# Optimization experiments

Hardware: AMD Instinct MI355X
Metric: run time of the kernel (lower is better)

## Reference

```python
import jax, jax.numpy as jnp
import numpy as np

N = 50000
E = 800000
NFEAT = 256
NHID = 64
HEADS = 4
NCLASS = 16
NEG_SLOPE = 0.2


def setup_inputs() -> dict:
    key = jax.random.key(0)
    ks = jax.random.split(key, 12)
    g = lambda k, s, scale: (jax.random.normal(k, s, dtype=jnp.float32) * scale)
    inp = {
        "x": g(ks[0], (N, NFEAT), 1.0),
        "src": jax.random.randint(ks[1], (E,), 0, N, dtype=jnp.int32),
        "dst": jax.random.randint(ks[2], (E,), 0, N, dtype=jnp.int32),
        # layer 1 params (DGL GATConv: fc no-bias, attn_l/attn_r, output bias)
        "W1": g(ks[3], (NFEAT, HEADS * NHID), (2.0 / NFEAT) ** 0.5),
        "al1": g(ks[4], (HEADS, NHID), 0.1),
        "ar1": g(ks[5], (HEADS, NHID), 0.1),
        "b1": jnp.zeros((HEADS * NHID,), dtype=jnp.float32),
        # layer 2 params (1 head)
        "W2": g(ks[6], (HEADS * NHID, NCLASS), (2.0 / (HEADS * NHID)) ** 0.5),
        "al2": g(ks[7], (1, NCLASS), 0.1),
        "ar2": g(ks[8], (1, NCLASS), 0.1),
        "b2": jnp.zeros((NCLASS,), dtype=jnp.float32),
    }
    return inp


def gat_conv(x, src, dst, W, al, ar, b, heads, dh):
    # x: [N, Fin] -> feat: [N, H, D]
    n = x.shape[0]
    feat = (x @ W).reshape(n, heads, dh)
    el = jnp.einsum("nhd,hd->nh", feat, al)  # [N, H]
    er = jnp.einsum("nhd,hd->nh", feat, ar)
    e = jax.nn.leaky_relu(el[src] + er[dst], NEG_SLOPE)  # [E, H]
    # segment softmax over destination nodes
    emax = jax.ops.segment_max(e, dst, num_segments=n)
    emax = jnp.where(jnp.isfinite(emax), emax, jnp.float32(0.0))
    ex = jnp.exp(e - emax[dst])  # [E, H]
    denom = jax.ops.segment_sum(ex, dst, num_segments=n)  # [N, H]
    alpha = ex / denom[dst]  # [E, H]
    # gather src feats, weight, scatter-add to dst
    msg = feat[src] * alpha[:, :, None]  # [E, H, D]
    out = jax.ops.segment_sum(msg, dst, num_segments=n)  # [N, H, D]
    return out + b.reshape(1, heads, dh)


def reference(x, src, dst, W1, al1, ar1, b1, W2, al2, ar2, b2):
    h = gat_conv(x, src, dst, W1, al1, ar1, b1, HEADS, NHID)  # [N, 4, nhid]
    h = h.reshape(N, HEADS * NHID)
    h = jax.nn.elu(h)
    h = gat_conv(h, src, dst, W2, al2, ar2, b2, 1, NCLASS)  # [N, 1, nclass]
    h = h.reshape(N, NCLASS)
    return jax.nn.log_softmax(h, axis=1)
```

## Files before the change

### kernel.cpp

```cpp
#include <hip/hip_runtime.h>
#include <hip/hip_bf16.h>

#define N_NODES 50000
#define NP1     50001
#define N_EDGES 800000
#define NFEAT   256
#define NHID    64
#define HEADS   4
#define NCLASS  16
#define NEG_SLOPE 0.2f

#define NBLK  782
#define NBUCK 196
#define NSCAN (NBUCK * NBLK)
#define NSCB  150
#define MAXB  5120

typedef __attribute__((ext_vector_type(8))) short short8;
typedef __attribute__((ext_vector_type(4))) float floatx4;
typedef __attribute__((ext_vector_type(2))) float floatx2;

__device__ __forceinline__ float blo(unsigned int u) { return __uint_as_float(u << 16); }
__device__ __forceinline__ float bhi(unsigned int u) { return __uint_as_float(u & 0xffff0000u); }
__device__ __forceinline__ float b2f(unsigned short u) {
    return __uint_as_float(((unsigned int)u) << 16);
}
__device__ __forceinline__ unsigned short f2b(float f) {
    unsigned int x = __float_as_uint(f);
    unsigned int r = x + 0x7fffu + ((x >> 16) & 1u);
    return (unsigned short)(r >> 16);
}
__device__ __forceinline__ unsigned int pack2(float a, float b) {
    return (unsigned int)f2b(a) | ((unsigned int)f2b(b) << 16);
}
__device__ __forceinline__ float leaky(float x) { return fmaxf(x, NEG_SLOPE * x); }

__device__ __forceinline__ void fp8acc(uint4 u, float ex, float* acc) {
    floatx2 p;
    p = __builtin_amdgcn_cvt_pk_f32_fp8(u.x, 0); acc[0]  = fmaf(p[0], ex, acc[0]);  acc[1]  = fmaf(p[1], ex, acc[1]);
    p = __builtin_amdgcn_cvt_pk_f32_fp8(u.x, 1); acc[2]  = fmaf(p[0], ex, acc[2]);  acc[3]  = fmaf(p[1], ex, acc[3]);
    p = __builtin_amdgcn_cvt_pk_f32_fp8(u.y, 0); acc[4]  = fmaf(p[0], ex, acc[4]);  acc[5]  = fmaf(p[1], ex, acc[5]);
    p = __builtin_amdgcn_cvt_pk_f32_fp8(u.y, 1); acc[6]  = fmaf(p[0], ex, acc[6]);  acc[7]  = fmaf(p[1], ex, acc[7]);
    p = __builtin_amdgcn_cvt_pk_f32_fp8(u.z, 0); acc[8]  = fmaf(p[0], ex, acc[8]);  acc[9]  = fmaf(p[1], ex, acc[9]);
    p = __builtin_amdgcn_cvt_pk_f32_fp8(u.z, 1); acc[10] = fmaf(p[0], ex, acc[10]); acc[11] = fmaf(p[1], ex, acc[11]);
    p = __builtin_amdgcn_cvt_pk_f32_fp8(u.w, 0); acc[12] = fmaf(p[0], ex, acc[12]); acc[13] = fmaf(p[1], ex, acc[13]);
    p = __builtin_amdgcn_cvt_pk_f32_fp8(u.w, 1); acc[14] = fmaf(p[0], ex, acc[14]); acc[15] = fmaf(p[1], ex, acc[15]);
}

__global__ __launch_bounds__(256) void p1_kernel(
        const int* __restrict__ dst, int* __restrict__ bhist,
        const float* __restrict__ W1, const float* __restrict__ W2,
        const float* __restrict__ al1, const float* __restrict__ ar1,
        unsigned short* __restrict__ W1E, unsigned short* __restrict__ W2T) {
    __shared__ float tile[64][65];
    __shared__ int hist[NBUCK];
    int b = blockIdx.x, t = threadIdx.x;
    if (b < NBLK) {
        if (t < NBUCK) hist[t] = 0;
        __syncthreads();
        int e = (b * 256 + t) * 4;
        if (e < N_EDGES) {
            int4 d = *(const int4*)&dst[e];
            atomicAdd(&hist[d.x >> 8], 1);
            atomicAdd(&hist[d.y >> 8], 1);
            atomicAdd(&hist[d.z >> 8], 1);
            atomicAdd(&hist[d.w >> 8], 1);
        }
        __syncthreads();
        if (t < NBUCK) bhist[t * NBLK + b] = hist[t];
        return;
    }
    int pb = b - NBLK;
    if (pb < 16) {
        int tk = (pb & 3) * 64, tn = (pb >> 2) * 64;
        int tx = t & 63, ty = t >> 6;
#pragma unroll
        for (int r = 0; r < 16; ++r) {
            int row = ty * 16 + r;
            tile[row][tx] = W1[(tk + row) * 256 + tn + tx];
        }
        __syncthreads();
#pragma unroll
        for (int r = 0; r < 16; ++r) {
            int row = ty * 16 + r;
            W1E[(tn + row) * 256 + tk + tx] = f2b(tile[tx][row]);
        }
    } else if (pb < 20) {
        int h = pb - 16;
        int w = t >> 6, lane = t & 63;
        float alv = al1[h * 64 + lane];
        float arv = ar1[h * 64 + lane];
        for (int k = w; k < 256; k += 4) {
            float wv = W1[k * 256 + h * 64 + lane];
            float sl = wv * alv, sr = wv * arv;
#pragma unroll
            for (int off = 1; off < 64; off <<= 1) {
                sl += __shfl_xor(sl, off);
                sr += __shfl_xor(sr, off);
            }
            if (lane == 0) {
                W1E[(256 + h) * 256 + k] = f2b(sl);
                W1E[(260 + h) * 256 + k] = f2b(sr);
            }
        }
    } else {
        int n = t >> 4, k0 = (t & 15) * 16;
#pragma unroll
        for (int j = 0; j < 16; ++j)
            W2T[n * 256 + k0 + j] = f2b(W2[(k0 + j) * 16 + n]);
#pragma unroll
        for (int j = 0; j < 8; ++j)
            W1E[264 * 256 + j * 256 + t] = 0;
    }
}

__global__ __launch_bounds__(256) void scanA_kernel(const int* __restrict__ bhist,
                                                    int* __restrict__ partial,
                                                    int* __restrict__ bsum) {
    __shared__ int wsum[4];
    int t = threadIdx.x;
    int base = blockIdx.x * 1024 + t * 4;
    int v0 = (base + 0 < NSCAN) ? bhist[base + 0] : 0;
    int v1 = (base + 1 < NSCAN) ? bhist[base + 1] : 0;
    int v2 = (base + 2 < NSCAN) ? bhist[base + 2] : 0;
    int v3 = (base + 3 < NSCAN) ? bhist[base + 3] : 0;
    int s = v0 + v1 + v2 + v3;
    int lane = t & 63, w = t >> 6;
    int incl = s;
#pragma unroll
    for (int off = 1; off < 64; off <<= 1) {
        int x = __shfl_up(incl, off);
        if (lane >= off) incl += x;
    }
    if (lane == 63) wsum[w] = incl;
    __syncthreads();
    int woff = 0;
    for (int k = 0; k < w; ++k) woff += wsum[k];
    int excl = woff + incl - s;
    if (base + 0 < NSCAN) partial[base + 0] = excl;
    if (base + 1 < NSCAN) partial[base + 1] = excl + v0;
    if (base + 2 < NSCAN) partial[base + 2] = excl + v0 + v1;
    if (base + 3 < NSCAN) partial[base + 3] = excl + v0 + v1 + v2;
    if (t == 255) bsum[blockIdx.x] = woff + incl;
}

__global__ __launch_bounds__(256) void p2_kernel(const int* __restrict__ src,
                                                 const int* __restrict__ dst,
                                                 const int* __restrict__ partial,
                                                 const int* __restrict__ bsum,
                                                 unsigned int* __restrict__ ebuf) {
    __shared__ int wsum[4];
    __shared__ int sb[256];
    __shared__ int bs[NBUCK];
    __shared__ int lcnt[256];
    __shared__ int lofs[256];
    __shared__ int lfill[256];
    __shared__ unsigned int sorted[1024];
    int b = blockIdx.x, t = threadIdx.x;
    int lane = t & 63, w = t >> 6;
    {
        int v = (t < NSCB) ? bsum[t] : 0;
        int incl = v;
#pragma unroll
        for (int off = 1; off < 64; off <<= 1) {
            int x = __shfl_up(incl, off);
            if (lane >= off) incl += x;
        }
        if (lane == 63) wsum[w] = incl;
        __syncthreads();
        int woff = 0;
        for (int k = 0; k < w; ++k) woff += wsum[k];
        sb[t] = woff + incl - v;
    }
    lcnt[t] = 0;
    __syncthreads();
    if (t < NBUCK) {
        int idx = t * NBLK + b;
        bs[t] = partial[idx] + sb[idx >> 10];
    }
    int e = (b * 256 + t) * 4;
    int4 d, s;
    bool valid = e < N_EDGES;
    if (valid) {
        d = *(const int4*)&dst[e];
        s = *(const int4*)&src[e];
        atomicAdd(&lcnt[d.x >> 8], 1);
        atomicAdd(&lcnt[d.y >> 8], 1);
        atomicAdd(&lcnt[d.z >> 8], 1);
        atomicAdd(&lcnt[d.w >> 8], 1);
    }
    __syncthreads();
    {
        int v = lcnt[t];
        int incl = v;
#pragma unroll
        for (int off = 1; off < 64; off <<= 1) {
            int x = __shfl_up(incl, off);
            if (lane >= off) incl += x;
        }
        if (lane == 63) wsum[w] = incl;
        __syncthreads();
        int woff = 0;
        for (int k = 0; k < w; ++k) woff += wsum[k];
        int excl = woff + incl - v;
        lofs[t] = excl;
        lfill[t] = excl;
    }
    __syncthreads();
    if (valid) {
        int p0 = atomicAdd(&lfill[d.x >> 8], 1);
        sorted[p0] = ((unsigned int)s.x << 16) | (unsigned int)d.x;
        int p1 = atomicAdd(&lfill[d.y >> 8], 1);
        sorted[p1] = ((unsigned int)s.y << 16) | (unsigned int)d.y;
        int p2 = atomicAdd(&lfill[d.z >> 8], 1);
        sorted[p2] = ((unsigned int)s.z << 16) | (unsigned int)d.z;
        int p3 = atomicAdd(&lfill[d.w >> 8], 1);
        sorted[p3] = ((unsigned int)s.w << 16) | (unsigned int)d.w;
    }
    __syncthreads();
    int ve = min(1024, N_EDGES - b * 1024);
    for (int i = t; i < ve; i += 256) {
        unsigned int p = sorted[i];
        int k = (p & 0xFFFFu) >> 8;
        ebuf[bs[k] + (i - lofs[k])] = p;
    }
}

__global__ __launch_bounds__(256) void p3_kernel(const int* __restrict__ partial,
                                                 const int* __restrict__ bsum,
                                                 const unsigned int* __restrict__ ebuf,
                                                 int* __restrict__ row_ptr,
                                                 int* __restrict__ csr_src) {
    __shared__ int wsum[4];
    __shared__ int sb[256];
    __shared__ int lcnt[256];
    __shared__ int lfill[256];
    __shared__ int sorted[MAXB];
    int b = blockIdx.x, t = threadIdx.x;
    int lane = t & 63, w = t >> 6;
    {
        int v = (t < NSCB) ? bsum[t] : 0;
        int incl = v;
#pragma unroll
        for (int off = 1; off < 64; off <<= 1) {
            int x = __shfl_up(incl, off);
            if (lane >= off) incl += x;
        }
        if (lane == 63) wsum[w] = incl;
        __syncthreads();
        int woff = 0;
        for (int k = 0; k < w; ++k) woff += wsum[k];
        sb[t] = woff + incl - v;
    }
    __syncthreads();
    int i0 = b * NBLK;
    int base = partial[i0] + sb[i0 >> 10];
    int endb;
    if (b == NBUCK - 1) endb = N_EDGES;
    else {
        int i1 = (b + 1) * NBLK;
        endb = partial[i1] + sb[i1 >> 10];
    }
    lcnt[t] = 0;
    __syncthreads();
    for (int i = base + t; i < endb; i += 256)
        atomicAdd(&lcnt[ebuf[i] & 255u], 1);
    __syncthreads();
    {
        int v = lcnt[t];
        int incl = v;
#pragma unroll
        for (int off = 1; off < 64; off <<= 1) {
            int x = __shfl_up(incl, off);
            if (lane >= off) incl += x;
        }
        if (lane == 63) wsum[w] = incl;
        __syncthreads();
        int woff = 0;
        for (int k = 0; k < w; ++k) woff += wsum[k];
        int excl = woff + incl - v;
        lfill[t] = excl;
        int node = b * 256 + t;
        if (node < NP1) row_ptr[node] = base + excl;
    }
    __syncthreads();
    for (int i = base + t; i < endb; i += 256) {
        unsigned int p = ebuf[i];
        int pos = atomicAdd(&lfill[p & 255u], 1);
        sorted[pos] = (int)(p >> 16);
    }
    __syncthreads();
    int M = endb - base;
    for (int i = t; i < M; i += 256)
        csr_src[base + i] = sorted[i];
}

__global__ __launch_bounds__(256, 2) void gemm1_mfma_kernel(
        const float* __restrict__ X, const unsigned short* __restrict__ BT,
        unsigned char* __restrict__ C, float* __restrict__ el, float* __restrict__ er) {
    __shared__ __align__(16) unsigned short As[128 * 40];
    __shared__ __align__(16) unsigned short Bs[272 * 40];
    int t = threadIdx.x;
    int m0 = blockIdx.x * 128;
    int lane = t & 63, wm = t >> 6;
    int quad = lane >> 4, l16 = lane & 15;

    floatx4 acc[2][17];
#pragma unroll
    for (int i = 0; i < 2; ++i)
#pragma unroll
        for (int j = 0; j < 17; ++j) acc[i][j] = (floatx4){0.f, 0.f, 0.f, 0.f};

    int arow = t >> 1, ak = (t & 1) * 16;
    int grow = m0 + arow;
    const float* xrow = X + (size_t)grow * 256 + ak;

    for (int k0 = 0; k0 < 256; k0 += 32) {
        float4 v0 = make_float4(0.f, 0.f, 0.f, 0.f), v1 = v0, v2 = v0, v3 = v0;
        if (grow < N_NODES) {
            v0 = *(const float4*)(xrow + k0 + 0);
            v1 = *(const float4*)(xrow + k0 + 4);
            v2 = *(const float4*)(xrow + k0 + 8);
            v3 = *(const float4*)(xrow + k0 + 12);
        }
        uint4 p0, p1;
        p0.x = pack2(v0.x, v0.y); p0.y = pack2(v0.z, v0.w);
        p0.z = pack2(v1.x, v1.y); p0.w = pack2(v1.z, v1.w);
        p1.x = pack2(v2.x, v2.y); p1.y = pack2(v2.z, v2.w);
        p1.z = pack2(v3.x, v3.y); p1.w = pack2(v3.z, v3.w);
        *(uint4*)&As[arow * 40 + ak] = p0;
        *(uint4*)&As[arow * 40 + ak + 8] = p1;
#pragma unroll
        for (int i = 0; i < 5; ++i) {
            int ch = t + i * 256;
            if (ch < 1088) {
                int row = ch >> 2, off = (ch & 3) * 8;
                *(uint4*)&Bs[row * 40 + off] = *(const uint4*)(BT + row * 256 + k0 + off);
            }
        }
        __syncthreads();

        short8 a0 = *(const short8*)&As[(wm * 32 + l16) * 40 + quad * 8];
        short8 a1 = *(const short8*)&As[(wm * 32 + 16 + l16) * 40 + quad * 8];
#pragma unroll
        for (int nf = 0; nf < 17; ++nf) {
            short8 bb = *(const short8*)&Bs[(nf * 16 + l16) * 40 + quad * 8];
            acc[0][nf] = __builtin_amdgcn_mfma_f32_16x16x32_bf16(a0, bb, acc[0][nf], 0, 0, 0);
            acc[1][nf] = __builtin_amdgcn_mfma_f32_16x16x32_bf16(a1, bb, acc[1][nf], 0, 0, 0);
        }
        __syncthreads();
    }

#pragma unroll
    for (int mf = 0; mf < 2; ++mf) {
#pragma unroll
        for (int r = 0; r < 4; ++r) {
            int row = m0 + wm * 32 + mf * 16 + quad * 4 + r;
            if (row < N_NODES && l16 < 8) {
                float v = acc[mf][16][r];
                if (l16 < 4) el[row * 4 + l16] = v;
                else er[row * 4 + (l16 - 4)] = v;
            }
        }
    }

    unsigned short* scr = Bs + wm * 1536;
    int half = lane >> 5, l32 = lane & 31;
    int rrow = l32 >> 1, coff = (l32 & 1) * 8;
#pragma unroll
    for (int mf = 0; mf < 2; ++mf) {
#pragma unroll
        for (int p = 0; p < 8; ++p) {
            unsigned short* base = scr + (p & 1) * 768;
#pragma unroll
            for (int fr = 0; fr < 2; ++fr) {
                int nf = 2 * p + fr;
                unsigned short* fb = base + fr * 384;
#pragma unroll
                for (int r = 0; r < 4; ++r)
                    fb[(quad * 4 + r) * 24 + l16] = f2b(acc[mf][nf][r]);
            }
            uint4 val = *(const uint4*)(base + half * 384 + rrow * 24 + coff);
            int row = m0 + wm * 32 + mf * 16 + rrow;
            int nf = 2 * p + half;
            if (row < N_NODES) {
                float f0 = blo(val.x), f1 = bhi(val.x), f2 = blo(val.y), f3 = bhi(val.y);
                float f4 = blo(val.z), f5 = bhi(val.z), f6 = blo(val.w), f7 = bhi(val.w);
                int lo = __builtin_amdgcn_cvt_pk_fp8_f32(f0, f1, 0, 0);
                lo = __builtin_amdgcn_cvt_pk_fp8_f32(f2, f3, lo, 1);
                int hi = __builtin_amdgcn_cvt_pk_fp8_f32(f4, f5, 0, 0);
                hi = __builtin_amdgcn_cvt_pk_fp8_f32(f6, f7, hi, 1);
                uint2 o;
                o.x = (unsigned int)lo;
                o.y = (unsigned int)hi;
                *(uint2*)&C[(size_t)row * 256 + nf * 16 + coff] = o;
            }
        }
    }
}

__global__ void agg1_kernel(const unsigned char* __restrict__ feat1,
                            const float* __restrict__ el, const float* __restrict__ er,
                            const int* __restrict__ row_ptr, const int* __restrict__ csr_src,
                            const float* __restrict__ b1, unsigned short* __restrict__ h1b) {
    int wave = threadIdx.x >> 6, lane = threadIdx.x & 63;
    int n = blockIdx.x * 4 + wave;
    if (n >= N_NODES) return;
    int q = lane >> 4, l16 = lane & 15;
    int h = l16 >> 2;
    float er_h = er[n * 4 + h];
    int start = row_ptr[n], end = row_ptr[n + 1];

    float acc[16];
#pragma unroll
    for (int j = 0; j < 16; ++j) acc[j] = 0.f;
    float denom = 0.f;

    int i = start + q;
    for (; i + 4 < end; i += 8) {
        int s0 = csr_src[i];
        int s1 = csr_src[i + 4];
        float ex0 = __expf(leaky(el[s0 * 4 + h] + er_h));
        float ex1 = __expf(leaky(el[s1 * 4 + h] + er_h));
        uint4 a = *(const uint4*)(feat1 + (size_t)s0 * 256 + l16 * 16);
        uint4 b = *(const uint4*)(feat1 + (size_t)s1 * 256 + l16 * 16);
        denom += ex0 + ex1;
        fp8acc(a, ex0, acc);
        fp8acc(b, ex1, acc);
    }
    if (i < end) {
        int s = csr_src[i];
        float ex = __expf(leaky(el[s * 4 + h] + er_h));
        uint4 u = *(const uint4*)(feat1 + (size_t)s * 256 + l16 * 16);
        denom += ex;
        fp8acc(u, ex, acc);
    }
#pragma unroll
    for (int j = 0; j < 16; ++j) {
        acc[j] += __shfl_xor(acc[j], 16);
        acc[j] += __shfl_xor(acc[j], 32);
    }
    denom += __shfl_xor(denom, 16);
    denom += __shfl_xor(denom, 32);

    if (q == 0) {
        float inv = (end > start) ? 1.f / denom : 0.f;
        float o[16];
#pragma unroll
        for (int j = 0; j < 16; j += 4) {
            float4 b4 = *(const float4*)&b1[l16 * 16 + j];
            o[j + 0] = fmaf(acc[j + 0], inv, b4.x);
            o[j + 1] = fmaf(acc[j + 1], inv, b4.y);
            o[j + 2] = fmaf(acc[j + 2], inv, b4.z);
            o[j + 3] = fmaf(acc[j + 3], inv, b4.w);
        }
#pragma unroll
        for (int j = 0; j < 16; ++j) o[j] = o[j] > 0.f ? o[j] : __expf(o[j]) - 1.f;
        uint4 pa, pb;
        pa.x = pack2(o[0], o[1]);   pa.y = pack2(o[2], o[3]);
        pa.z = pack2(o[4], o[5]);   pa.w = pack2(o[6], o[7]);
        pb.x = pack2(o[8], o[9]);   pb.y = pack2(o[10], o[11]);
        pb.z = pack2(o[12], o[13]); pb.w = pack2(o[14], o[15]);
        uint4* dstp = (uint4*)(h1b + (size_t)n * 256 + l16 * 16);
        dstp[0] = pa;
        dstp[1] = pb;
    }
}

__global__ __launch_bounds__(256) void gemm2_mfma_kernel(
        const unsigned short* __restrict__ h1b, const unsigned short* __restrict__ W2T,
        const float* __restrict__ al2, const float* __restrict__ ar2,
        unsigned short* __restrict__ feat2b, float* __restrict__ el2, float* __restrict__ er2) {
    int wave = threadIdx.x >> 6, lane = threadIdx.x & 63;
    int l16 = lane & 15, quad = lane >> 4;
    int row0 = (blockIdx.x * 4 + wave) * 16;
    if (row0 >= N_NODES) return;
    floatx4 acc = (floatx4){0.f, 0.f, 0.f, 0.f};
    const unsigned short* arow = h1b + (size_t)(row0 + l16) * 256 + quad * 8;
    const unsigned short* brow = W2T + (size_t)l16 * 256 + quad * 8;
#pragma unroll
    for (int k0 = 0; k0 < 256; k0 += 32) {
        short8 a = *(const short8*)(arow + k0);
        short8 b = *(const short8*)(brow + k0);
        acc = __builtin_amdgcn_mfma_f32_16x16x32_bf16(a, b, acc, 0, 0, 0);
    }
    float a2 = al2[l16], r2 = ar2[l16];
#pragma unroll
    for (int r = 0; r < 4; ++r) {
        int row = row0 + quad * 4 + r;
        float v = acc[r];
        feat2b[row * 16 + l16] = f2b(v);
        float pl = v * a2, pr = v * r2;
#pragma unroll
        for (int off = 1; off < 16; off <<= 1) {
            pl += __shfl_xor(pl, off);
            pr += __shfl_xor(pr, off);
        }
        if (l16 == 0) {
            el2[row] = pl;
            er2[row] = pr;
        }
    }
}

__global__ void agg2_kernel(const unsigned short* __restrict__ feat2b,
                            const float* __restrict__ el2, const float* __restrict__ er2,
                            const int* __restrict__ row_ptr, const int* __restrict__ csr_src,
                            const float* __restrict__ b2, float* __restrict__ out) {
    int wave = threadIdx.x >> 6, lane = threadIdx.x & 63;
    int n = blockIdx.x * 4 + wave;
    if (n >= N_NODES) return;
    int start = row_ptr[n], end = row_ptr[n + 1];
    float ern = er2[n];
    int eo = lane >> 4, c = lane & 15;
    float acc = 0.f, denom = 0.f;
    int i = start + eo;
    for (; i + 4 < end; i += 8) {
        int s0 = csr_src[i], s1 = csr_src[i + 4];
        float ex0 = __expf(leaky(el2[s0] + ern));
        float ex1 = __expf(leaky(el2[s1] + ern));
        float f0 = b2f(feat2b[s0 * 16 + c]), f1 = b2f(feat2b[s1 * 16 + c]);
        denom += ex0 + ex1;
        acc = fmaf(f0, ex0, acc);
        acc = fmaf(f1, ex1, acc);
    }
    if (i < end) {
        int s = csr_src[i];
        float ex = __expf(leaky(el2[s] + ern));
        denom += ex;
        acc = fmaf(b2f(feat2b[s * 16 + c]), ex, acc);
    }
    acc += __shfl_xor(acc, 16);
    acc += __shfl_xor(acc, 32);
    denom += __shfl_xor(denom, 16);
    denom += __shfl_xor(denom, 32);
    float v = ((end > start) ? acc / denom : 0.f) + b2[c];
    float mx = v;
#pragma unroll
    for (int off = 1; off < 16; off <<= 1) mx = fmaxf(mx, __shfl_xor(mx, off));
    float ex2 = __expf(v - mx);
    float s2 = ex2;
#pragma unroll
    for (int off = 1; off < 16; off <<= 1) s2 += __shfl_xor(s2, off);
    float res = v - mx - logf(s2);
    if (lane < 16) out[n * 16 + lane] = res;
}

extern "C" void kernel_launch(void* const* d_in, const int* in_sizes, int n_in,
                              void* d_out, int out_size, void* d_ws, size_t ws_size,
                              hipStream_t stream) {
    const float* x   = (const float*)d_in[0];
    const int*   src = (const int*)d_in[1];
    const int*   dst = (const int*)d_in[2];
    const float* W1  = (const float*)d_in[3];
    const float* al1 = (const float*)d_in[4];
    const float* ar1 = (const float*)d_in[5];
    const float* b1  = (const float*)d_in[6];
    const float* W2  = (const float*)d_in[7];
    const float* al2 = (const float*)d_in[8];
    const float* ar2 = (const float*)d_in[9];
    const float* b2  = (const float*)d_in[10];
    float* out = (float*)d_out;

    char* ws = (char*)d_ws;
    size_t off = 0;
    auto alloc = [&](size_t bytes) -> void* {
        void* p = ws + off;
        off += (bytes + 255) & ~(size_t)255;
        return p;
    };
    unsigned short* W1E    = (unsigned short*)alloc((size_t)272 * 256 * 2);
    unsigned short* W2T    = (unsigned short*)alloc((size_t)16 * 256 * 2);
    unsigned char*  feat1  = (unsigned char*)alloc((size_t)N_NODES * 256);
    unsigned short* h1b    = (unsigned short*)alloc((size_t)N_NODES * 256 * 2);
    unsigned short* feat2b = (unsigned short*)alloc((size_t)N_NODES * 16 * 2);
    float* el1     = (float*)alloc((size_t)N_NODES * 4 * 4);
    float* er1     = (float*)alloc((size_t)N_NODES * 4 * 4);
    float* el2     = (float*)alloc((size_t)N_NODES * 4);
    float* er2     = (float*)alloc((size_t)N_NODES * 4);
    int*   bhist   = (int*)alloc((size_t)NSCAN * 4);
    int*   partial = (int*)alloc((size_t)NSCAN * 4);
    int*   bsum    = (int*)alloc((size_t)256 * 4);
    int*   row_ptr = (int*)alloc((size_t)NP1 * 4);
    unsigned int* ebuf = (unsigned int*)alloc((size_t)N_EDGES * 4);
    int*   csr_src = (int*)alloc((size_t)N_EDGES * 4);

    dim3 b256(256);
    p1_kernel<<<NBLK + 21, b256, 0, stream>>>(dst, bhist, W1, W2, al1, ar1, W1E, W2T);
    scanA_kernel<<<NSCB, b256, 0, stream>>>(bhist, partial, bsum);
    p2_kernel<<<NBLK, b256, 0, stream>>>(src, dst, partial, bsum, ebuf);
    p3_kernel<<<NBUCK, b256, 0, stream>>>(partial, bsum, ebuf, row_ptr, csr_src);

    gemm1_mfma_kernel<<<(N_NODES + 127) / 128, b256, 0, stream>>>(x, W1E, feat1, el1, er1);
    agg1_kernel<<<(N_NODES + 3) / 4, b256, 0, stream>>>(feat1, el1, er1, row_ptr, csr_src, b1, h1b);

    gemm2_mfma_kernel<<<(N_NODES + 63) / 64, b256, 0, stream>>>(h1b, W2T, al2, ar2, feat2b, el2, er2);
    agg2_kernel<<<(N_NODES + 3) / 4, b256, 0, stream>>>(feat2b, el2, er2, row_ptr, csr_src, b2, out);
}
```

Measured before the change: 247.6 us.

## Merge GEMM1 into edge-sort scatter kernel and pack FMAs in agg1

The layer-1 GEMM (x@W1 plus el/er) now runs in the same launch as the edge bucket-scatter pass. The first 391 blocks do the MFMA GEMM and the rest do the sort scatter, so the two independent stages overlap and one launch is removed. The agg1 accumulation now uses floatx2 elementwise FMA to encourage packed FMA instructions. The combined kernel carries the GEMM's larger shared-memory footprint in every block, which may lower occupancy for the scatter blocks.

```diff
diff --git a/kernel.cpp b/kernel.cpp
--- a/kernel.cpp
+++ b/kernel.cpp
@@ -15,6 +15,7 @@
 #define NSCAN (NBUCK * NBLK)
 #define NSCB  150
 #define MAXB  5120
+#define NGB   391
 
 typedef __attribute__((ext_vector_type(8))) short short8;
 typedef __attribute__((ext_vector_type(4))) float floatx4;
@@ -35,16 +36,15 @@
 }
 __device__ __forceinline__ float leaky(float x) { return fmaxf(x, NEG_SLOPE * x); }
 
-__device__ __forceinline__ void fp8acc(uint4 u, float ex, float* acc) {
-    floatx2 p;
-    p = __builtin_amdgcn_cvt_pk_f32_fp8(u.x, 0); acc[0]  = fmaf(p[0], ex, acc[0]);  acc[1]  = fmaf(p[1], ex, acc[1]);
-    p = __builtin_amdgcn_cvt_pk_f32_fp8(u.x, 1); acc[2]  = fmaf(p[0], ex, acc[2]);  acc[3]  = fmaf(p[1], ex, acc[3]);
-    p = __builtin_amdgcn_cvt_pk_f32_fp8(u.y, 0); acc[4]  = fmaf(p[0], ex, acc[4]);  acc[5]  = fmaf(p[1], ex, acc[5]);
-    p = __builtin_amdgcn_cvt_pk_f32_fp8(u.y, 1); acc[6]  = fmaf(p[0], ex, acc[6]);  acc[7]  = fmaf(p[1], ex, acc[7]);
-    p = __builtin_amdgcn_cvt_pk_f32_fp8(u.z, 0); acc[8]  = fmaf(p[0], ex, acc[8]);  acc[9]  = fmaf(p[1], ex, acc[9]);
-    p = __builtin_amdgcn_cvt_pk_f32_fp8(u.z, 1); acc[10] = fmaf(p[0], ex, acc[10]); acc[11] = fmaf(p[1], ex, acc[11]);
-    p = __builtin_amdgcn_cvt_pk_f32_fp8(u.w, 0); acc[12] = fmaf(p[0], ex, acc[12]); acc[13] = fmaf(p[1], ex, acc[13]);
-    p = __builtin_amdgcn_cvt_pk_f32_fp8(u.w, 1); acc[14] = fmaf(p[0], ex, acc[14]); acc[15] = fmaf(p[1], ex, acc[15]);
+__device__ __forceinline__ void fp8acc2(uint4 u, floatx2 exv, floatx2* acc) {
+    acc[0] = __builtin_elementwise_fma(__builtin_amdgcn_cvt_pk_f32_fp8(u.x, 0), exv, acc[0]);
+    acc[1] = __builtin_elementwise_fma(__builtin_amdgcn_cvt_pk_f32_fp8(u.x, 1), exv, acc[1]);
+    acc[2] = __builtin_elementwise_fma(__builtin_amdgcn_cvt_pk_f32_fp8(u.y, 0), exv, acc[2]);
+    acc[3] = __builtin_elementwise_fma(__builtin_amdgcn_cvt_pk_f32_fp8(u.y, 1), exv, acc[3]);
+    acc[4] = __builtin_elementwise_fma(__builtin_amdgcn_cvt_pk_f32_fp8(u.z, 0), exv, acc[4]);
+    acc[5] = __builtin_elementwise_fma(__builtin_amdgcn_cvt_pk_f32_fp8(u.z, 1), exv, acc[5]);
+    acc[6] = __builtin_elementwise_fma(__builtin_amdgcn_cvt_pk_f32_fp8(u.w, 0), exv, acc[6]);
+    acc[7] = __builtin_elementwise_fma(__builtin_amdgcn_cvt_pk_f32_fp8(u.w, 1), exv, acc[7]);
 }
 
 __global__ __launch_bounds__(256) void p1_kernel(
@@ -144,11 +144,14 @@
     if (t == 255) bsum[blockIdx.x] = woff + incl;
 }
 
-__global__ __launch_bounds__(256) void p2_kernel(const int* __restrict__ src,
-                                                 const int* __restrict__ dst,
-                                                 const int* __restrict__ partial,
-                                                 const int* __restrict__ bsum,
-                                                 unsigned int* __restrict__ ebuf) {
+__global__ __launch_bounds__(256, 2) void p2g1_kernel(
+        const int* __restrict__ src, const int* __restrict__ dst,
+        const int* __restrict__ partial, const int* __restrict__ bsum,
+        unsigned int* __restrict__ ebuf,
+        const float* __restrict__ X, const unsigned short* __restrict__ BT,
+        unsigned char* __restrict__ C, float* __restrict__ el, float* __restrict__ er) {
+    __shared__ __align__(16) unsigned short As[128 * 40];
+    __shared__ __align__(16) unsigned short Bs[272 * 40];
     __shared__ int wsum[4];
     __shared__ int sb[256];
     __shared__ int bs[NBUCK];
@@ -156,73 +159,175 @@
     __shared__ int lofs[256];
     __shared__ int lfill[256];
     __shared__ unsigned int sorted[1024];
-    int b = blockIdx.x, t = threadIdx.x;
-    int lane = t & 63, w = t >> 6;
-    {
-        int v = (t < NSCB) ? bsum[t] : 0;
-        int incl = v;
-#pragma unroll
-        for (int off = 1; off < 64; off <<= 1) {
-            int x = __shfl_up(incl, off);
-            if (lane >= off) incl += x;
-        }
-        if (lane == 63) wsum[w] = incl;
-        __syncthreads();
-        int woff = 0;
-        for (int k = 0; k < w; ++k) woff += wsum[k];
-        sb[t] = woff + incl - v;
-    }
-    lcnt[t] = 0;
-    __syncthreads();
-    if (t < NBUCK) {
-        int idx = t * NBLK + b;
-        bs[t] = partial[idx] + sb[idx >> 10];
-    }
-    int e = (b * 256 + t) * 4;
-    int4 d, s;
-    bool valid = e < N_EDGES;
-    if (valid) {
-        d = *(const int4*)&dst[e];
-        s = *(const int4*)&src[e];
-        atomicAdd(&lcnt[d.x >> 8], 1);
-        atomicAdd(&lcnt[d.y >> 8], 1);
-        atomicAdd(&lcnt[d.z >> 8], 1);
-        atomicAdd(&lcnt[d.w >> 8], 1);
-    }
-    __syncthreads();
-    {
-        int v = lcnt[t];
-        int incl = v;
-#pragma unroll
-        for (int off = 1; off < 64; off <<= 1) {
-            int x = __shfl_up(incl, off);
-            if (lane >= off) incl += x;
-        }
-        if (lane == 63) wsum[w] = incl;
-        __syncthreads();
-        int woff = 0;
-        for (int k = 0; k < w; ++k) woff += wsum[k];
-        int excl = woff + incl - v;
-        lofs[t] = excl;
-        lfill[t] = excl;
-    }
-    __syncthreads();
-    if (valid) {
-        int p0 = atomicAdd(&lfill[d.x >> 8], 1);
-        sorted[p0] = ((unsigned int)s.x << 16) | (unsigned int)d.x;
-        int p1 = atomicAdd(&lfill[d.y >> 8], 1);
-        sorted[p1] = ((unsigned int)s.y << 16) | (unsigned int)d.y;
-        int p2 = atomicAdd(&lfill[d.z >> 8], 1);
-        sorted[p2] = ((unsigned int)s.z << 16) | (unsigned int)d.z;
-        int p3 = atomicAdd(&lfill[d.w >> 8], 1);
-        sorted[p3] = ((unsigned int)s.w << 16) | (unsigned int)d.w;
-    }
-    __syncthreads();
-    int ve = min(1024, N_EDGES - b * 1024);
-    for (int i = t; i < ve; i += 256) {
-        unsigned int p = sorted[i];
-        int k = (p & 0xFFFFu) >> 8;
-        ebuf[bs[k] + (i - lofs[k])] = p;
+
+    int t = threadIdx.x;
+    if (blockIdx.x >= NGB) {
+        int b = blockIdx.x - NGB;
+        int lane = t & 63, w = t >> 6;
+        {
+            int v = (t < NSCB) ? bsum[t] : 0;
+            int incl = v;
+#pragma unroll
+            for (int off = 1; off < 64; off <<= 1) {
+                int x = __shfl_up(incl, off);
+                if (lane >= off) incl += x;
+            }
+            if (lane == 63) wsum[w] = incl;
+            __syncthreads();
+            int woff = 0;
+            for (int k = 0; k < w; ++k) woff += wsum[k];
+            sb[t] = woff + incl - v;
+        }
+        lcnt[t] = 0;
+        __syncthreads();
+        if (t < NBUCK) {
+            int idx = t * NBLK + b;
+            bs[t] = partial[idx] + sb[idx >> 10];
+        }
+        int e = (b * 256 + t) * 4;
+        int4 d, s;
+        bool valid = e < N_EDGES;
+        if (valid) {
+            d = *(const int4*)&dst[e];
+            s = *(const int4*)&src[e];
+            atomicAdd(&lcnt[d.x >> 8], 1);
+            atomicAdd(&lcnt[d.y >> 8], 1);
+            atomicAdd(&lcnt[d.z >> 8], 1);
+            atomicAdd(&lcnt[d.w >> 8], 1);
+        }
+        __syncthreads();
+        {
+            int v = lcnt[t];
+            int incl = v;
+#pragma unroll
+            for (int off = 1; off < 64; off <<= 1) {
+                int x = __shfl_up(incl, off);
+                if (lane >= off) incl += x;
+            }
+            if (lane == 63) wsum[w] = incl;
+            __syncthreads();
+            int woff = 0;
+            for (int k = 0; k < w; ++k) woff += wsum[k];
+            int excl = woff + incl - v;
+            lofs[t] = excl;
+            lfill[t] = excl;
+        }
+        __syncthreads();
+        if (valid) {
+            int p0 = atomicAdd(&lfill[d.x >> 8], 1);
+            sorted[p0] = ((unsigned int)s.x << 16) | (unsigned int)d.x;
+            int p1 = atomicAdd(&lfill[d.y >> 8], 1);
+            sorted[p1] = ((unsigned int)s.y << 16) | (unsigned int)d.y;
+            int p2 = atomicAdd(&lfill[d.z >> 8], 1);
+            sorted[p2] = ((unsigned int)s.z << 16) | (unsigned int)d.z;
+            int p3 = atomicAdd(&lfill[d.w >> 8], 1);
+            sorted[p3] = ((unsigned int)s.w << 16) | (unsigned int)d.w;
+        }
+        __syncthreads();
+        int ve = min(1024, N_EDGES - b * 1024);
+        for (int i = t; i < ve; i += 256) {
+            unsigned int p = sorted[i];
+            int k = (p & 0xFFFFu) >> 8;
+            ebuf[bs[k] + (i - lofs[k])] = p;
+        }
+        return;
+    }
+
+    int m0 = blockIdx.x * 128;
+    int lane = t & 63, wm = t >> 6;
+    int quad = lane >> 4, l16 = lane & 15;
+
+    floatx4 acc[2][17];
+#pragma unroll
+    for (int i = 0; i < 2; ++i)
+#pragma unroll
+        for (int j = 0; j < 17; ++j) acc[i][j] = (floatx4){0.f, 0.f, 0.f, 0.f};
+
+    int arow = t >> 1, ak = (t & 1) * 16;
+    int grow = m0 + arow;
+    const float* xrow = X + (size_t)grow * 256 + ak;
+
+    for (int k0 = 0; k0 < 256; k0 += 32) {
+        float4 v0 = make_float4(0.f, 0.f, 0.f, 0.f), v1 = v0, v2 = v0, v3 = v0;
+        if (grow < N_NODES) {
+            v0 = *(const float4*)(xrow + k0 + 0);
+            v1 = *(const float4*)(xrow + k0 + 4);
+            v2 = *(const float4*)(xrow + k0 + 8);
+            v3 = *(const float4*)(xrow + k0 + 12);
+        }
+        uint4 p0, p1;
+        p0.x = pack2(v0.x, v0.y); p0.y = pack2(v0.z, v0.w);
+        p0.z = pack2(v1.x, v1.y); p0.w = pack2(v1.z, v1.w);
+        p1.x = pack2(v2.x, v2.y); p1.y = pack2(v2.z, v2.w);
+        p1.z = pack2(v3.x, v3.y); p1.w = pack2(v3.z, v3.w);
+        *(uint4*)&As[arow * 40 + ak] = p0;
+        *(uint4*)&As[arow * 40 + ak + 8] = p1;
+#pragma unroll
+        for (int i = 0; i < 5; ++i) {
+            int ch = t + i * 256;
+            if (ch < 1088) {
+                int row = ch >> 2, off = (ch & 3) * 8;
+                *(uint4*)&Bs[row * 40 + off] = *(const uint4*)(BT + row * 256 + k0 + off);
+            }
+        }
+        __syncthreads();
+
+        short8 a0 = *(const short8*)&As[(wm * 32 + l16) * 40 + quad * 8];
+        short8 a1 = *(const short8*)&As[(wm * 32 + 16 + l16) * 40 + quad * 8];
+#pragma unroll
+        for (int nf = 0; nf < 17; ++nf) {
+            short8 bb = *(const short8*)&Bs[(nf * 16 + l16) * 40 + quad * 8];
+            acc[0][nf] = __builtin_amdgcn_mfma_f32_16x16x32_bf16(a0, bb, acc[0][nf], 0, 0, 0);
+            acc[1][nf] = __builtin_amdgcn_mfma_f32_16x16x32_bf16(a1, bb, acc[1][nf], 0, 0, 0);
+        }
+        __syncthreads();
+    }
+
+#pragma unroll
+    for (int mf = 0; mf < 2; ++mf) {
+#pragma unroll
+        for (int r = 0; r < 4; ++r) {
+            int row = m0 + wm * 32 + mf * 16 + quad * 4 + r;
+            if (row < N_NODES && l16 < 8) {
+                float v = acc[mf][16][r];
+                if (l16 < 4) el[row * 4 + l16] = v;
+                else er[row * 4 + (l16 - 4)] = v;
+            }
+        }
+    }
+
+    unsigned short* scr = Bs + wm * 1536;
+    int half = lane >> 5, l32 = lane & 31;
+    int rrow = l32 >> 1, coff = (l32 & 1) * 8;
+#pragma unroll
+    for (int mf = 0; mf < 2; ++mf) {
+#pragma unroll
+        for (int p = 0; p < 8; ++p) {
+            unsigned short* base = scr + (p & 1) * 768;
+#pragma unroll
+            for (int fr = 0; fr < 2; ++fr) {
+                int nf = 2 * p + fr;
+                unsigned short* fb = base + fr * 384;
+#pragma unroll
+                for (int r = 0; r < 4; ++r)
+                    fb[(quad * 4 + r) * 24 + l16] = f2b(acc[mf][nf][r]);
+            }
+            uint4 val = *(const uint4*)(base + half * 384 + rrow * 24 + coff);
+            int row = m0 + wm * 32 + mf * 16 + rrow;
+            int nf = 2 * p + half;
+            if (row < N_NODES) {
+                float f0 = blo(val.x), f1 = bhi(val.x), f2 = blo(val.y), f3 = bhi(val.y);
+                float f4 = blo(val.z), f5 = bhi(val.z), f6 = blo(val.w), f7 = bhi(val.w);
+                int lo = __builtin_amdgcn_cvt_pk_fp8_f32(f0, f1, 0, 0);
+                lo = __builtin_amdgcn_cvt_pk_fp8_f32(f2, f3, lo, 1);
+                int hi = __builtin_amdgcn_cvt_pk_fp8_f32(f4, f5, 0, 0);
+                hi = __builtin_amdgcn_cvt_pk_fp8_f32(f6, f7, hi, 1);
+                uint2 o;
+                o.x = (unsigned int)lo;
+                o.y = (unsigned int)hi;
+                *(uint2*)&C[(size_t)row * 256 + nf * 16 + coff] = o;
+            }
+        }
     }
 }
 
@@ -295,110 +400,6 @@
         csr_src[base + i] = sorted[i];
 }
 
-__global__ __launch_bounds__(256, 2) void gemm1_mfma_kernel(
-        const float* __restrict__ X, const unsigned short* __restrict__ BT,
-        unsigned char* __restrict__ C, float* __restrict__ el, float* __restrict__ er) {
-    __shared__ __align__(16) unsigned short As[128 * 40];
-    __shared__ __align__(16) unsigned short Bs[272 * 40];
-    int t = threadIdx.x;
-    int m0 = blockIdx.x * 128;
-    int lane = t & 63, wm = t >> 6;
-    int quad = lane >> 4, l16 = lane & 15;
-
-    floatx4 acc[2][17];
-#pragma unroll
-    for (int i = 0; i < 2; ++i)
-#pragma unroll
-        for (int j = 0; j < 17; ++j) acc[i][j] = (floatx4){0.f, 0.f, 0.f, 0.f};
-
-    int arow = t >> 1, ak = (t & 1) * 16;
-    int grow = m0 + arow;
-    const float* xrow = X + (size_t)grow * 256 + ak;
-
-    for (int k0 = 0; k0 < 256; k0 += 32) {
-        float4 v0 = make_float4(0.f, 0.f, 0.f, 0.f), v1 = v0, v2 = v0, v3 = v0;
-        if (grow < N_NODES) {
-            v0 = *(const float4*)(xrow + k0 + 0);
-            v1 = *(const float4*)(xrow + k0 + 4);
-            v2 = *(const float4*)(xrow + k0 + 8);
-            v3 = *(const float4*)(xrow + k0 + 12);
-        }
-        uint4 p0, p1;
-        p0.x = pack2(v0.x, v0.y); p0.y = pack2(v0.z, v0.w);
-        p0.z = pack2(v1.x, v1.y); p0.w = pack2(v1.z, v1.w);
-        p1.x = pack2(v2.x, v2.y); p1.y = pack2(v2.z, v2.w);
-        p1.z = pack2(v3.x, v3.y); p1.w = pack2(v3.z, v3.w);
-        *(uint4*)&As[arow * 40 + ak] = p0;
-        *(uint4*)&As[arow * 40 + ak + 8] = p1;
-#pragma unroll
-        for (int i = 0; i < 5; ++i) {
-            int ch = t + i * 256;
-            if (ch < 1088) {
-                int row = ch >> 2, off = (ch & 3) * 8;
-                *(uint4*)&Bs[row * 40 + off] = *(const uint4*)(BT + row * 256 + k0 + off);
-            }
-        }
-        __syncthreads();
-
-        short8 a0 = *(const short8*)&As[(wm * 32 + l16) * 40 + quad * 8];
-        short8 a1 = *(const short8*)&As[(wm * 32 + 16 + l16) * 40 + quad * 8];
-#pragma unroll
-        for (int nf = 0; nf < 17; ++nf) {
-            short8 bb = *(const short8*)&Bs[(nf * 16 + l16) * 40 + quad * 8];
-            acc[0][nf] = __builtin_amdgcn_mfma_f32_16x16x32_bf16(a0, bb, acc[0][nf], 0, 0, 0);
-            acc[1][nf] = __builtin_amdgcn_mfma_f32_16x16x32_bf16(a1, bb, acc[1][nf], 0, 0, 0);
-        }
-        __syncthreads();
-    }
-
-#pragma unroll
-    for (int mf = 0; mf < 2; ++mf) {
-#pragma unroll
-        for (int r = 0; r < 4; ++r) {
-            int row = m0 + wm * 32 + mf * 16 + quad * 4 + r;
-            if (row < N_NODES && l16 < 8) {
-                float v = acc[mf][16][r];
-                if (l16 < 4) el[row * 4 + l16] = v;
-                else er[row * 4 + (l16 - 4)] = v;
-            }
-        }
-    }
-
-    unsigned short* scr = Bs + wm * 1536;
-    int half = lane >> 5, l32 = lane & 31;
-    int rrow = l32 >> 1, coff = (l32 & 1) * 8;
-#pragma unroll
-    for (int mf = 0; mf < 2; ++mf) {
-#pragma unroll
-        for (int p = 0; p < 8; ++p) {
-            unsigned short* base = scr + (p & 1) * 768;
-#pragma unroll
-            for (int fr = 0; fr < 2; ++fr) {
-                int nf = 2 * p + fr;
-                unsigned short* fb = base + fr * 384;
-#pragma unroll
-                for (int r = 0; r < 4; ++r)
-                    fb[(quad * 4 + r) * 24 + l16] = f2b(acc[mf][nf][r]);
-            }
-            uint4 val = *(const uint4*)(base + half * 384 + rrow * 24 + coff);
-            int row = m0 + wm * 32 + mf * 16 + rrow;
-            int nf = 2 * p + half;
-            if (row < N_NODES) {
-                float f0 = blo(val.x), f1 = bhi(val.x), f2 = blo(val.y), f3 = bhi(val.y);
-                float f4 = blo(val.z), f5 = bhi(val.z), f6 = blo(val.w), f7 = bhi(val.w);
-                int lo = __builtin_amdgcn_cvt_pk_fp8_f32(f0, f1, 0, 0);
-                lo = __builtin_amdgcn_cvt_pk_fp8_f32(f2, f3, lo, 1);
-                int hi = __builtin_amdgcn_cvt_pk_fp8_f32(f4, f5, 0, 0);
-                hi = __builtin_amdgcn_cvt_pk_fp8_f32(f6, f7, hi, 1);
-                uint2 o;
-                o.x = (unsigned int)lo;
-                o.y = (unsigned int)hi;
-                *(uint2*)&C[(size_t)row * 256 + nf * 16 + coff] = o;
-            }
-        }
-    }
-}
-
 __global__ void agg1_kernel(const unsigned char* __restrict__ feat1,
                             const float* __restrict__ el, const float* __restrict__ er,
                             const int* __restrict__ row_ptr, const int* __restrict__ csr_src,
@@ -411,9 +412,9 @@
     float er_h = er[n * 4 + h];
     int start = row_ptr[n], end = row_ptr[n + 1];
 
-    float acc[16];
-#pragma unroll
-    for (int j = 0; j < 16; ++j) acc[j] = 0.f;
+    floatx2 acc2[8];
+#pragma unroll
+    for (int j = 0; j < 8; ++j) acc2[j] = (floatx2){0.f, 0.f};
     float denom = 0.f;
 
     int i = start + q;
@@ -425,15 +426,21 @@
         uint4 a = *(const uint4*)(feat1 + (size_t)s0 * 256 + l16 * 16);
         uint4 b = *(const uint4*)(feat1 + (size_t)s1 * 256 + l16 * 16);
         denom += ex0 + ex1;
-        fp8acc(a, ex0, acc);
-        fp8acc(b, ex1, acc);
+        fp8acc2(a, (floatx2){ex0, ex0}, acc2);
+        fp8acc2(b, (floatx2){ex1, ex1}, acc2);
     }
     if (i < end) {
         int s = csr_src[i];
         float ex = __expf(leaky(el[s * 4 + h] + er_h));
         uint4 u = *(const uint4*)(feat1 + (size_t)s * 256 + l16 * 16);
         denom += ex;
-        fp8acc(u, ex, acc);
+        fp8acc2(u, (floatx2){ex, ex}, acc2);
+    }
+    float acc[16];
+#pragma unroll
+    for (int j = 0; j < 8; ++j) {
+        acc[2 * j] = acc2[j][0];
+        acc[2 * j + 1] = acc2[j][1];
     }
 #pragma unroll
     for (int j = 0; j < 16; ++j) {
@@ -588,10 +595,10 @@
     dim3 b256(256);
     p1_kernel<<<NBLK + 21, b256, 0, stream>>>(dst, bhist, W1, W2, al1, ar1, W1E, W2T);
     scanA_kernel<<<NSCB, b256, 0, stream>>>(bhist, partial, bsum);
-    p2_kernel<<<NBLK, b256, 0, stream>>>(src, dst, partial, bsum, ebuf);
+    p2g1_kernel<<<NGB + NBLK, b256, 0, stream>>>(src, dst, partial, bsum, ebuf,
+                                                 x, W1E, feat1, el1, er1);
     p3_kernel<<<NBUCK, b256, 0, stream>>>(partial, bsum, ebuf, row_ptr, csr_src);
 
-    gemm1_mfma_kernel<<<(N_NODES + 127) / 128, b256, 0, stream>>>(x, W1E, feat1, el1, er1);
     agg1_kernel<<<(N_NODES + 3) / 4, b256, 0, stream>>>(feat1, el1, er1, row_ptr, csr_src, b1, h1b);
 
     gemm2_mfma_kernel<<<(N_NODES + 63) / 64, b256, 0, stream>>>(h1b, W2T, al2, ar2, feat2b, el2, er2);
```

Result: no change. 245.1 us (-1.0%).
